# Kernel optimization log

Hardware: AMD Instinct MI355X
Metric: run time of the kernel (lower is better)

## Reference

```python
import jax, jax.numpy as jnp
import numpy as np

N, E, B = 10000, 160000, 64
ND, ED, H, L, C = 128, 64, 256, 4, 10
LN_EPS = 1e-5


def _layernorm(x, g, b):
    mu = jnp.mean(x, axis=-1, keepdims=True)
    var = jnp.mean(jnp.square(x - mu), axis=-1, keepdims=True)
    return (x - mu) * jax.lax.rsqrt(var + LN_EPS) * g + b


def setup_inputs() -> dict:
    key = jax.random.key(0)
    ks = jax.random.split(key, 24)

    def w(k, shape, fan_in):
        return jax.random.normal(k, shape, jnp.float32) * (1.0 / np.sqrt(fan_in))

    node_features = jax.random.normal(ks[0], (N, ND), jnp.float32)
    edge_index = jax.random.randint(ks[1], (2, E), 0, N, jnp.int64)
    edge_features = jax.random.normal(ks[2], (E, ED), jnp.float32)
    # deterministic sorted batch assignment (no empty graphs)
    batch = (jnp.arange(N, dtype=jnp.int64) * B) // N

    inp = dict(
        node_features=node_features,
        edge_index=edge_index,
        edge_features=edge_features,
        batch=batch,
        node_W=w(ks[3], (ND, H), ND), node_b=jnp.zeros((H,), jnp.float32),
        edge_W=w(ks[4], (ED, H), ED), edge_b=jnp.zeros((H,), jnp.float32),
        msg_W1=w(ks[5], (L, 3 * H, H), 3 * H), msg_b1=jnp.zeros((L, H), jnp.float32),
        msg_W2=w(ks[6], (L, H, H), H), msg_b2=jnp.zeros((L, H), jnp.float32),
        upd_W1=w(ks[7], (L, 2 * H, H), 2 * H), upd_b1=jnp.zeros((L, H), jnp.float32),
        upd_W2=w(ks[8], (L, H, H), H), upd_b2=jnp.zeros((L, H), jnp.float32),
        ln_g=jnp.ones((L, H), jnp.float32), ln_b=jnp.zeros((L, H), jnp.float32),
        ro_W1=w(ks[9], (H, H), H), ro_b1=jnp.zeros((H,), jnp.float32),
        ro_W2=w(ks[10], (H, C), H), ro_b2=jnp.zeros((C,), jnp.float32),
    )
    return inp


def _forward(node_features, edge_features, node_W, node_b, edge_W, edge_b,
             msg_W1, msg_b1, msg_W2, msg_b2, upd_W1, upd_b1, upd_W2, upd_b2,
             ln_g, ln_b, ro_W1, ro_b1, ro_W2, ro_b2, edge_index, batch):
    src, dst = edge_index[0], edge_index[1]
    x = node_features @ node_W + node_b            # [N, H]
    edge_attr = edge_features @ edge_W + edge_b    # [E, H]
    for l in range(L):
        # batched gather-MLP over all edges (vectorized version of the per-edge loop)
        m_in = jnp.concatenate([x[src], x[dst], edge_attr], axis=-1)  # [E, 3H]
        msg = jax.nn.relu(m_in @ msg_W1[l] + msg_b1[l]) @ msg_W2[l] + msg_b2[l]
        agg = jnp.zeros_like(x).at[dst].add(msg)    # scatter-add by destination
        u_in = jnp.concatenate([x, agg], axis=-1)   # [N, 2H]
        upd = jax.nn.relu(u_in @ upd_W1[l] + upd_b1[l]) @ upd_W2[l] + upd_b2[l]
        x = _layernorm(x + upd, ln_g[l], ln_b[l])
    # global mean pool per graph
    sums = jax.ops.segment_sum(x, batch, num_segments=B)
    cnts = jax.ops.segment_sum(jnp.ones((x.shape[0], 1), x.dtype), batch, num_segments=B)
    pooled = sums / cnts                            # [B, H]
    return jax.nn.relu(pooled @ ro_W1 + ro_b1) @ ro_W2 + ro_b2  # [B, C]


def reference(node_features, edge_index, edge_features, batch,
              node_W, node_b, edge_W, edge_b,
              msg_W1, msg_b1, msg_W2, msg_b2,
              upd_W1, upd_b1, upd_W2, upd_b2,
              ln_g, ln_b, ro_W1, ro_b1, ro_W2, ro_b2):
    return _forward(node_features, edge_features, node_W, node_b, edge_W, edge_b,
                    msg_W1, msg_b1, msg_W2, msg_b2, upd_W1, upd_b1, upd_W2, upd_b2,
                    ln_g, ln_b, ro_W1, ro_b1, ro_W2, ro_b2, edge_index, batch)
```

## Files before the change

kernel.cpp:

```cpp
#include <hip/hip_runtime.h>
#include <cstdint>
#include <cstddef>


typedef unsigned short u16;
typedef __attribute__((ext_vector_type(4))) float f32x4;
typedef __attribute__((ext_vector_type(8))) short bf16x8;
typedef __attribute__((ext_vector_type(4))) short s16x4;

constexpr int kN  = 10000;
constexpr int kE  = 160000;
constexpr int kB  = 64;
constexpr int kH  = 256;
constexpr int kL  = 4;
constexpr int kC  = 10;
constexpr float kEps = 1e-5f;

struct __align__(16) F4 { float v[4]; };
__device__ __forceinline__ F4 ldF4(const float* p) { return *reinterpret_cast<const F4*>(p); }

__device__ __forceinline__ u16 f2bf(float f) {
    unsigned u = __builtin_bit_cast(unsigned, f);
    return (u16)((u + 0x7fffu + ((u >> 16) & 1u)) >> 16);
}
__device__ __forceinline__ float bf2f(u16 h) {
    return __builtin_bit_cast(float, (unsigned)h << 16);
}

typedef __attribute__((address_space(1))) void GV;
typedef __attribute__((address_space(3))) void LV;
__device__ __forceinline__ void gl_lds16(const void* g, void* l) {
    __builtin_amdgcn_global_load_lds((GV*)g, (LV*)l, 16, 0, 0);
}
__device__ __forceinline__ void dma_w16k(const u16* __restrict__ Wc, char* lds, int tid) {
    const int w = tid >> 6, lane = tid & 63;
    char* lb = lds + w * 4096;
    const char* gb = (const char*)Wc + w * 4096 + lane * 16;
    #pragma unroll
    for (int i = 0; i < 4; ++i) gl_lds16(gb + i * 1024, lb + i * 1024);
}

__global__ void k_detect_i64(const unsigned* __restrict__ w, int* __restrict__ flag) {
    if (threadIdx.x == 0 && blockIdx.x == 0) {
        int is64 = 1;
        for (int i = 0; i < 64; ++i)
            if (w[2*i + 1] != 0u) { is64 = 0; break; }
        *flag = is64;
    }
}
__global__ void k_cvt_idx(const unsigned* __restrict__ w, const int* __restrict__ flag,
                          int* __restrict__ out, int n) {
    int i = blockIdx.x * 256 + threadIdx.x;
    if (i < n) out[i] = (*flag) ? (int)w[2*i] : (int)w[i];
}

__global__ __launch_bounds__(256) void k_hist(const int* __restrict__ dst,
                                              int* __restrict__ cnt) {
    int e = blockIdx.x * 256 + threadIdx.x;
    if (e < kE) atomicAdd(&cnt[dst[e]], 1);
}
__global__ __launch_bounds__(256) void k_scan(const int* __restrict__ cnt,
                                              int* __restrict__ cur) {
    __shared__ int part[256];
    const int t = threadIdx.x;
    const int per = (kN + 255) / 256;
    int s = 0;
    for (int i = 0; i < per; ++i) {
        int idx = t * per + i;
        if (idx < kN) s += cnt[idx];
    }
    int own = s;
    part[t] = s; __syncthreads();
    for (int off = 1; off < 256; off <<= 1) {
        int v = (t >= off) ? part[t - off] : 0;
        __syncthreads();
        part[t] += v;
        __syncthreads();
    }
    int run = part[t] - own;
    for (int i = 0; i < per; ++i) {
        int idx = t * per + i;
        if (idx < kN) { cur[idx] = run; run += cnt[idx]; }
    }
}
__global__ __launch_bounds__(256) void k_scatter(
    const int* __restrict__ src, const int* __restrict__ dst,
    int* __restrict__ cur, int* __restrict__ perm,
    int* __restrict__ ssorted, int* __restrict__ dsorted) {
    int e = blockIdx.x * 256 + threadIdx.x;
    if (e < kE) {
        int d = dst[e];
        int p = atomicAdd(&cur[d], 1);
        perm[p] = e;
        ssorted[p] = src[e];
        dsorted[p] = d;
    }
}

__global__ __launch_bounds__(256) void k_prep_w(
    const float* __restrict__ mW1, const float* __restrict__ mW2,
    const float* __restrict__ uW1, const float* __restrict__ uW2,
    u16* __restrict__ tm1, u16* __restrict__ tm2,
    u16* __restrict__ tu1, u16* __restrict__ tu2)
{
    int idx = blockIdx.x * 256 + threadIdx.x;
    const int S1 = kL * 768 * 256;
    const int S2 = S1 + kL * 256 * 256;
    const int S3 = S2 + kL * 512 * 256;
    const int S4 = S3 + kL * 256 * 256;
    const float* src; u16* dst; int K, r;
    if (idx < S1)      { src = mW1; dst = tm1; K = 768; r = idx; }
    else if (idx < S2) { src = mW2; dst = tm2; K = 256; r = idx - S1; }
    else if (idx < S3) { src = uW1; dst = tu1; K = 512; r = idx - S2; }
    else if (idx < S4) { src = uW2; dst = tu2; K = 256; r = idx - S3; }
    else return;
    int per = K * 256;
    int layer = r / per, rr = r - layer * per;
    int k = rr >> 8, n = rr & 255;
    int kc = k >> 5, kg = (k >> 3) & 3, e = k & 7;
    dst[(size_t)layer * per + (size_t)kc * 8192 + n * 32 + ((kg ^ ((n >> 1) & 3)) << 3) + e]
        = f2bf(src[(size_t)layer * per + rr]);
}

__global__ __launch_bounds__(256) void k_prep_m(
    const float* __restrict__ eW, const float* __restrict__ eb,
    const float* __restrict__ mW1, const float* __restrict__ mb1,
    u16* __restrict__ tmc, float* __restrict__ b1p)
{
    __shared__ float sWe[16 * 256];
    const int l = blockIdx.x, rq = blockIdx.y, t = threadIdx.x;
    const int r0 = rq * 16;
    #pragma unroll
    for (int i = 0; i < 16; ++i) sWe[i * 256 + t] = eW[(size_t)(r0 + i) * 256 + t];
    __syncthreads();
    const float* W1c = mW1 + (size_t)l * 768 * 256 + (size_t)512 * 256;
    float m[16];
    #pragma unroll
    for (int r = 0; r < 16; ++r) m[r] = 0.f;
    float bp = (rq == 0) ? mb1[l * 256 + t] : 0.f;
    for (int j = 0; j < 256; ++j) {
        float wv = W1c[(size_t)j * 256 + t];
        if (rq == 0) bp = fmaf(eb[j], wv, bp);
        #pragma unroll
        for (int r = 0; r < 16; ++r) m[r] = fmaf(sWe[r * 256 + j], wv, m[r]);
    }
    if (rq == 0) b1p[l * 256 + t] = bp;
    #pragma unroll
    for (int r = 0; r < 16; ++r) {
        int k = r0 + r;
        int kc = k >> 5, kg = (k >> 3) & 3, e = k & 7;
        tmc[(size_t)l * 16384 + (size_t)kc * 8192 + t * 32
            + ((kg ^ ((t >> 1) & 3)) << 3) + e] = f2bf(m[r]);
    }
}

__global__ __launch_bounds__(256) void k_encode_nodes(
    const float* __restrict__ nf, const float* __restrict__ W,
    const float* __restrict__ b, float* __restrict__ x, u16* __restrict__ x_bf)
{
    __shared__ float s_nf[4 * 128];
    const int n0 = blockIdx.x * 4;
    const int tid = threadIdx.x;
    reinterpret_cast<float2*>(s_nf)[tid] =
        reinterpret_cast<const float2*>(nf + (size_t)n0 * 128)[tid];
    __syncthreads();
    float acc[4] = {0.f, 0.f, 0.f, 0.f};
    for (int k = 0; k < 128; ++k) {
        float w = W[k * kH + tid];
        #pragma unroll
        for (int r = 0; r < 4; ++r) acc[r] = fmaf(s_nf[r * 128 + k], w, acc[r]);
    }
    float bias = b[tid];
    #pragma unroll
    for (int r = 0; r < 4; ++r) {
        float o = acc[r] + bias;
        x[(size_t)(n0 + r) * kH + tid] = o;
        x_bf[(size_t)(n0 + r) * kH + tid] = f2bf(o);
    }
}

__device__ __forceinline__ bf16x8 rdfrag(const char* lds, int n, int kg) {
    return *reinterpret_cast<const bf16x8*>(lds + n * 64 + ((kg ^ ((n >> 1) & 3)) << 4));
}
__device__ __forceinline__ bf16x8 rdH(const char* H, int row, int kbyte) {
    return *reinterpret_cast<const bf16x8*>(H + row * 512 + (kbyte ^ ((row & 7) << 4)));
}

__global__ __launch_bounds__(256, 3) void k_node_pre(
    const u16* __restrict__ x_bf, const u16* __restrict__ Wt1,
    u16* __restrict__ y_a, u16* __restrict__ y_b)
{
    __shared__ char sWt[16384];
    __shared__ char sA[4096];
    const int tid = threadIdx.x;
    const int n0 = blockIdx.x * 64;
    const int half = blockIdx.y;
    const u16* Wt = Wt1 + (size_t)half * 8 * 8192;
    u16* y = half ? y_b : y_a;
    const int w = tid >> 6, lane = tid & 63;
    const int lr = lane & 15, lg = lane >> 4;
    const int srow = tid >> 2, skg = tid & 3;
    const int kg_src = skg ^ ((srow >> 1) & 3);
    int gnode = n0 + srow; if (gnode >= kN) gnode = kN - 1;

    f32x4 acc[4][4];
    #pragma unroll
    for (int i = 0; i < 4; ++i)
        #pragma unroll
        for (int j = 0; j < 4; ++j) acc[i][j] = (f32x4){0.f, 0.f, 0.f, 0.f};

    for (int kc = 0; kc < 8; ++kc) {
        __syncthreads();
        dma_w16k(Wt + (size_t)kc * 8192, sWt, tid);
        gl_lds16(x_bf + (size_t)gnode * kH + kc * 32 + kg_src * 8, sA + w * 1024);
        __syncthreads();
        bf16x8 af[4], bfm[4];
        #pragma unroll
        for (int i = 0; i < 4; ++i) af[i] = rdfrag(sWt, w * 64 + i * 16 + lr, lg);
        #pragma unroll
        for (int j = 0; j < 4; ++j) bfm[j] = rdfrag(sA, j * 16 + lr, lg);
        #pragma unroll
        for (int i = 0; i < 4; ++i)
            #pragma unroll
            for (int j = 0; j < 4; ++j)
                acc[i][j] = __builtin_amdgcn_mfma_f32_16x16x32_bf16(af[i], bfm[j], acc[i][j], 0, 0, 0);
    }
    #pragma unroll
    for (int i = 0; i < 4; ++i) {
        const int hc0 = w * 64 + i * 16 + lg * 4;
        #pragma unroll
        for (int j = 0; j < 4; ++j) {
            const int node = n0 + j * 16 + lr;
            if (node < kN) {
                s16x4 o;
                #pragma unroll
                for (int q = 0; q < 4; ++q) o[q] = (short)f2bf(acc[i][j][q]);
                *reinterpret_cast<s16x4*>(y + (size_t)node * kH + hc0) = o;
            }
        }
    }
}

__global__ __launch_bounds__(256, 3) void k_msg(
    const float* __restrict__ ef,
    const int* __restrict__ ssorted, const int* __restrict__ dsorted,
    const int* __restrict__ perm,
    const u16* __restrict__ y_a, const u16* __restrict__ y_b,
    const u16* __restrict__ Wtm, const float* __restrict__ b1p,
    const u16* __restrict__ Wt2, const float* __restrict__ b2,
    float* __restrict__ agg)
{
    __shared__ char sWt[16384];
    __shared__ char sA[4096];
    __shared__ char sH[32768];
    __shared__ int sDst[64];

    const int tid = threadIdx.x;
    const int nwg = gridDim.x;
    const int q8 = nwg >> 3, r8 = nwg & 7;
    const int xcd = blockIdx.x & 7, sub = blockIdx.x >> 3;
    const int bid = (xcd < r8 ? xcd * (q8 + 1) : r8 * (q8 + 1) + (xcd - r8) * q8) + sub;
    const int e0 = bid * 64;

    const int w = tid >> 6, lane = tid & 63;
    const int lr = lane & 15, lg = lane >> 4;
    const int srow = tid >> 2, skg = tid & 3;

    const int my_src  = ssorted[e0 + srow];
    const int my_dst  = dsorted[e0 + srow];
    const int my_perm = perm[e0 + srow];
    if (tid < 64) sDst[tid] = dsorted[e0 + tid];

    #pragma unroll
    for (int m = 0; m < 8; ++m) {
        int col0 = skg * 8 + m * 32;
        bf16x8 va = *reinterpret_cast<const bf16x8*>(y_a + (size_t)my_src * kH + col0);
        bf16x8 vb = *reinterpret_cast<const bf16x8*>(y_b + (size_t)my_dst * kH + col0);
        bf16x8 o;
        #pragma unroll
        for (int t = 0; t < 8; ++t)
            o[t] = (short)f2bf(bf2f((u16)va[t]) + bf2f((u16)vb[t]));
        int byte = srow * 512 + col0 * 2;
        *reinterpret_cast<bf16x8*>(sH + (byte ^ ((srow & 7) << 4))) = o;
    }

    f32x4 acc[4][4];
    #pragma unroll
    for (int i = 0; i < 4; ++i)
        #pragma unroll
        for (int j = 0; j < 4; ++j) acc[i][j] = (f32x4){0.f, 0.f, 0.f, 0.f};

    for (int kc = 0; kc < 2; ++kc) {
        __syncthreads();
        dma_w16k(Wtm + (size_t)kc * 8192, sWt, tid);
        {
            const float* ap = ef + (size_t)my_perm * 64 + kc * 32 + skg * 8;
            F4 a0 = ldF4(ap), a1 = ldF4(ap + 4);
            int4 bv;
            bv.x = (int)f2bf(a0.v[0]) | ((int)f2bf(a0.v[1]) << 16);
            bv.y = (int)f2bf(a0.v[2]) | ((int)f2bf(a0.v[3]) << 16);
            bv.z = (int)f2bf(a1.v[0]) | ((int)f2bf(a1.v[1]) << 16);
            bv.w = (int)f2bf(a1.v[2]) | ((int)f2bf(a1.v[3]) << 16);
            *reinterpret_cast<int4*>(sA + srow * 64 + ((skg ^ ((srow >> 1) & 3)) << 4)) = bv;
        }
        __syncthreads();
        bf16x8 af[4], bfm[4];
        #pragma unroll
        for (int i = 0; i < 4; ++i) af[i] = rdfrag(sWt, w * 64 + i * 16 + lr, lg);
        #pragma unroll
        for (int j = 0; j < 4; ++j) bfm[j] = rdfrag(sA, j * 16 + lr, lg);
        #pragma unroll
        for (int i = 0; i < 4; ++i)
            #pragma unroll
            for (int j = 0; j < 4; ++j)
                acc[i][j] = __builtin_amdgcn_mfma_f32_16x16x32_bf16(af[i], bfm[j], acc[i][j], 0, 0, 0);
    }

    #pragma unroll
    for (int i = 0; i < 4; ++i) {
        const int hc0 = w * 64 + i * 16 + lg * 4;
        const F4 bb = ldF4(b1p + hc0);
        #pragma unroll
        for (int j = 0; j < 4; ++j) {
            const int edge = j * 16 + lr;
            int addr = (edge * 512 + hc0 * 2) ^ ((edge & 7) << 4);
            s16x4 ys = *reinterpret_cast<const s16x4*>(sH + addr);
            s16x4 o;
            #pragma unroll
            for (int q = 0; q < 4; ++q) {
                float h = acc[i][j][q] + bb.v[q] + bf2f((u16)ys[q]);
                h = h > 0.f ? h : 0.f;
                o[q] = (short)f2bf(h);
            }
            *reinterpret_cast<s16x4*>(sH + addr) = o;
            acc[i][j] = (f32x4){0.f, 0.f, 0.f, 0.f};
        }
    }

    for (int kc = 0; kc < 8; ++kc) {
        __syncthreads();
        dma_w16k(Wt2 + (size_t)kc * 8192, sWt, tid);
        __syncthreads();
        bf16x8 af2[4], bf2[4];
        #pragma unroll
        for (int i = 0; i < 4; ++i) af2[i] = rdH(sH, i * 16 + lr, kc * 64 + lg * 16);
        #pragma unroll
        for (int j = 0; j < 4; ++j) bf2[j] = rdfrag(sWt, w * 64 + j * 16 + lr, lg);
        #pragma unroll
        for (int i = 0; i < 4; ++i)
            #pragma unroll
            for (int j = 0; j < 4; ++j)
                acc[i][j] = __builtin_amdgcn_mfma_f32_16x16x32_bf16(af2[i], bf2[j], acc[i][j], 0, 0, 0);
    }

    __syncthreads();
    #pragma unroll
    for (int j = 0; j < 4; ++j) {
        const int oc = w * 64 + j * 16 + lr;
        const float b2v = b2[oc];
        #pragma unroll
        for (int i = 0; i < 4; ++i)
            #pragma unroll
            for (int q = 0; q < 4; ++q) {
                int edge = i * 16 + lg * 4 + q;
                int byte = edge * 512 + oc * 2;
                *reinterpret_cast<u16*>(sH + (byte ^ ((edge & 7) << 4)))
                    = f2bf(acc[i][j][q] + b2v);
            }
    }
    __syncthreads();

    {
        const int col = tid;
        float run = 0.f;
        int prev = sDst[0];
        #pragma unroll 1
        for (int eb = 0; eb < 8; ++eb) {
            float vv[8]; int dd[8];
            #pragma unroll
            for (int t = 0; t < 8; ++t) {
                int e = eb * 8 + t;
                int byte = e * 512 + col * 2;
                vv[t] = bf2f(*reinterpret_cast<const u16*>(sH + (byte ^ ((e & 7) << 4))));
                dd[t] = sDst[e];
            }
            #pragma unroll
            for (int t = 0; t < 8; ++t) {
                if (dd[t] != prev) {
                    unsafeAtomicAdd(agg + (size_t)prev * kH + col, run);
                    run = 0.f; prev = dd[t];
                }
                run += vv[t];
            }
        }
        unsafeAtomicAdd(agg + (size_t)prev * kH + col, run);
    }
}

__global__ __launch_bounds__(256, 2) void k_upd(
    float* __restrict__ x, u16* __restrict__ x_bf,
    float* __restrict__ agg,
    const u16* __restrict__ Wt1, const float* __restrict__ b1,
    const u16* __restrict__ Wt2, const float* __restrict__ b2,
    const float* __restrict__ lng, const float* __restrict__ lnb)
{
    __shared__ char sWt[2][16384];
    __shared__ char sA[2][4096];
    __shared__ char sH[32768];

    const int tid = threadIdx.x;
    const int n0 = blockIdx.x * 64;
    const int w = tid >> 6, lane = tid & 63;
    const int lr = lane & 15, lg = lane >> 4;
    const int srow = tid >> 2, skg = tid & 3;
    const int kg_src = skg ^ ((srow >> 1) & 3);
    int gnode = n0 + srow; if (gnode >= kN) gnode = kN - 1;

    dma_w16k(Wt1, sWt[0], tid);
    gl_lds16(x_bf + (size_t)gnode * kH + kg_src * 8, sA[0] + w * 1024);

    f32x4 acc[4][4];
    #pragma unroll
    for (int i = 0; i < 4; ++i)
        #pragma unroll
        for (int j = 0; j < 4; ++j) acc[i][j] = (f32x4){0.f, 0.f, 0.f, 0.f};
    __syncthreads();

    for (int kc = 0; kc < 16; ++kc) {
        const int cur = kc & 1, nxt = cur ^ 1;
        bool do_agg = false; F4 a0, a1;
        if (kc < 15) {
            dma_w16k(Wt1 + (size_t)(kc + 1) * 8192, sWt[nxt], tid);
            if (kc + 1 < 8) {
                gl_lds16(x_bf + (size_t)gnode * kH + (kc + 1) * 32 + kg_src * 8,
                         sA[nxt] + w * 1024);
            } else {
                const float* ap = agg + (size_t)gnode * kH + (kc + 1 - 8) * 32 + skg * 8;
                a0 = ldF4(ap); a1 = ldF4(ap + 4); do_agg = true;
            }
        } else {
            dma_w16k(Wt2, sWt[nxt], tid);
        }
        bf16x8 af[4], bfm[4];
        #pragma unroll
        for (int i = 0; i < 4; ++i) af[i] = rdfrag(sWt[cur], w * 64 + i * 16 + lr, lg);
        #pragma unroll
        for (int j = 0; j < 4; ++j) bfm[j] = rdfrag(sA[cur], j * 16 + lr, lg);
        #pragma unroll
        for (int i = 0; i < 4; ++i)
            #pragma unroll
            for (int j = 0; j < 4; ++j)
                acc[i][j] = __builtin_amdgcn_mfma_f32_16x16x32_bf16(af[i], bfm[j], acc[i][j], 0, 0, 0);
        if (do_agg) {
            int4 bv;
            bv.x = (int)f2bf(a0.v[0]) | ((int)f2bf(a0.v[1]) << 16);
            bv.y = (int)f2bf(a0.v[2]) | ((int)f2bf(a0.v[3]) << 16);
            bv.z = (int)f2bf(a1.v[0]) | ((int)f2bf(a1.v[1]) << 16);
            bv.w = (int)f2bf(a1.v[2]) | ((int)f2bf(a1.v[3]) << 16);
            *reinterpret_cast<int4*>(sA[nxt] + srow * 64 + ((skg ^ ((srow >> 1) & 3)) << 4)) = bv;
        }
        __syncthreads();
    }

    #pragma unroll
    for (int i = 0; i < 4; ++i) {
        const int hc0 = w * 64 + i * 16 + lg * 4;
        const F4 bb = ldF4(b1 + hc0);
        #pragma unroll
        for (int j = 0; j < 4; ++j) {
            const int row = j * 16 + lr;
            s16x4 o;
            #pragma unroll
            for (int q = 0; q < 4; ++q) {
                float h = acc[i][j][q] + bb.v[q];
                h = h > 0.f ? h : 0.f;
                o[q] = (short)f2bf(h);
            }
            int byte = row * 512 + hc0 * 2;
            *reinterpret_cast<s16x4*>(sH + (byte ^ ((row & 7) << 4))) = o;
            acc[i][j] = (f32x4){0.f, 0.f, 0.f, 0.f};
        }
    }
    __syncthreads();

    {
        float4 z = make_float4(0.f, 0.f, 0.f, 0.f);
        float4* bp = reinterpret_cast<float4*>(agg + (size_t)n0 * kH);
        #pragma unroll
        for (int i = 0; i < 16; ++i) {
            int idx = i * 256 + tid;
            int row = idx >> 6;
            if (n0 + row < kN) bp[idx] = z;
        }
    }

    for (int kc = 0; kc < 8; ++kc) {
        const int cur = kc & 1, nxt = cur ^ 1;
        if (kc < 7) dma_w16k(Wt2 + (size_t)(kc + 1) * 8192, sWt[nxt], tid);
        bf16x8 af2[4], bf2[4];
        #pragma unroll
        for (int i = 0; i < 4; ++i) af2[i] = rdH(sH, i * 16 + lr, kc * 64 + lg * 16);
        #pragma unroll
        for (int j = 0; j < 4; ++j) bf2[j] = rdfrag(sWt[cur], w * 64 + j * 16 + lr, lg);
        #pragma unroll
        for (int i = 0; i < 4; ++i)
            #pragma unroll
            for (int j = 0; j < 4; ++j)
                acc[i][j] = __builtin_amdgcn_mfma_f32_16x16x32_bf16(af2[i], bf2[j], acc[i][j], 0, 0, 0);
        __syncthreads();
    }

    float b2v[4], gv[4], bvn[4];
    #pragma unroll
    for (int j = 0; j < 4; ++j) {
        int oc = w * 64 + j * 16 + lr;
        b2v[j] = b2[oc]; gv[j] = lng[oc]; bvn[j] = lnb[oc];
    }
    #pragma unroll
    for (int i = 0; i < 4; ++i)
        #pragma unroll
        for (int j = 0; j < 4; ++j) {
            int oc = w * 64 + j * 16 + lr;
            #pragma unroll
            for (int q = 0; q < 4; ++q) {
                int node = n0 + i * 16 + lg * 4 + q;
                int ncl = node < kN ? node : kN - 1;
                acc[i][j][q] += b2v[j] + x[(size_t)ncl * kH + oc];
            }
        }

    float (*red)[64][2] = reinterpret_cast<float(*)[64][2]>(sA[0]);
    float2* mstd = reinterpret_cast<float2*>(sA[0] + 2048);
    __syncthreads();
    #pragma unroll
    for (int i = 0; i < 4; ++i)
        #pragma unroll
        for (int q = 0; q < 4; ++q) {
            float s = acc[i][0][q] + acc[i][1][q] + acc[i][2][q] + acc[i][3][q];
            float ss = acc[i][0][q] * acc[i][0][q] + acc[i][1][q] * acc[i][1][q]
                     + acc[i][2][q] * acc[i][2][q] + acc[i][3][q] * acc[i][3][q];
            #pragma unroll
            for (int m = 1; m < 16; m <<= 1) { s += __shfl_xor(s, m); ss += __shfl_xor(ss, m); }
            if (lr == 0) { red[w][i * 16 + lg * 4 + q][0] = s; red[w][i * 16 + lg * 4 + q][1] = ss; }
        }
    __syncthreads();
    if (tid < 64) {
        float s = red[0][tid][0] + red[1][tid][0] + red[2][tid][0] + red[3][tid][0];
        float ss = red[0][tid][1] + red[1][tid][1] + red[2][tid][1] + red[3][tid][1];
        float mean = s * (1.f / 256.f);
        float var = ss * (1.f / 256.f) - mean * mean;
        mstd[tid] = make_float2(mean, rsqrtf(var + kEps));
    }
    __syncthreads();
    #pragma unroll
    for (int i = 0; i < 4; ++i)
        #pragma unroll
        for (int j = 0; j < 4; ++j) {
            int oc = w * 64 + j * 16 + lr;
            #pragma unroll
            for (int q = 0; q < 4; ++q) {
                int nn = i * 16 + lg * 4 + q;
                int node = n0 + nn;
                if (node < kN) {
                    float2 ms = mstd[nn];
                    float o = (acc[i][j][q] - ms.x) * ms.y * gv[j] + bvn[j];
                    x[(size_t)node * kH + oc] = o;
                    x_bf[(size_t)node * kH + oc] = f2bf(o);
                }
            }
        }
}

__device__ __forceinline__ int lower_bound_i(const int* a, int n, int v) {
    int lo = 0, hi = n;
    while (lo < hi) { int m = (lo + hi) >> 1; if (a[m] < v) lo = m + 1; else hi = m; }
    return lo;
}

__global__ __launch_bounds__(256) void k_pool_ro(
    const float* __restrict__ x, const int* __restrict__ batch,
    const float* __restrict__ W1, const float* __restrict__ b1,
    const float* __restrict__ W2, const float* __restrict__ b2,
    float* __restrict__ out)
{
    __shared__ float ph[kH];
    __shared__ float h1[kH];
    const int b = blockIdx.x, t = threadIdx.x;
    const int s = lower_bound_i(batch, kN, b);
    const int e = lower_bound_i(batch, kN, b + 1);
    float acc = 0.f;
    for (int i = s; i < e; ++i) acc += x[(size_t)i * kH + t];
    ph[t] = acc / (float)(e - s);
    __syncthreads();
    float a = b1[t];
    for (int k = 0; k < kH; ++k) a = fmaf(ph[k], W1[k * kH + t], a);
    h1[t] = a > 0.f ? a : 0.f;
    __syncthreads();
    if (t < kC) {
        float o = b2[t];
        for (int k = 0; k < kH; ++k) o = fmaf(h1[k], W2[k * kC + t], o);
        out[b * kC + t] = o;
    }
}

extern "C" void kernel_launch(void* const* d_in, const int* in_sizes, int n_in,
                              void* d_out, int out_size, void* d_ws, size_t ws_size,
                              hipStream_t stream)
{
    const float* nf     = (const float*)d_in[0];
    const void*  ei_raw = d_in[1];
    const float* ef     = (const float*)d_in[2];
    const void*  ba_raw = d_in[3];
    const float* node_W = (const float*)d_in[4];
    const float* node_b = (const float*)d_in[5];
    const float* edge_W = (const float*)d_in[6];
    const float* edge_b = (const float*)d_in[7];
    const float* msg_W1 = (const float*)d_in[8];
    const float* msg_b1 = (const float*)d_in[9];
    const float* msg_W2 = (const float*)d_in[10];
    const float* msg_b2 = (const float*)d_in[11];
    const float* upd_W1 = (const float*)d_in[12];
    const float* upd_b1 = (const float*)d_in[13];
    const float* upd_W2 = (const float*)d_in[14];
    const float* upd_b2 = (const float*)d_in[15];
    const float* ln_g   = (const float*)d_in[16];
    const float* ln_b   = (const float*)d_in[17];
    const float* ro_W1  = (const float*)d_in[18];
    const float* ro_b1  = (const float*)d_in[19];
    const float* ro_W2  = (const float*)d_in[20];
    const float* ro_b2  = (const float*)d_in[21];

    char* p = (char*)d_ws;
    auto alloc = [&](size_t bytes) { char* r = p; p += (bytes + 255) & ~(size_t)255; return r; };
    float* x    = (float*)alloc((size_t)kN * kH * 4);
    float* agg  = (float*)alloc((size_t)kN * kH * 4);
    u16* x_bf   = (u16*)alloc((size_t)kN * kH * 2);
    u16* y_a    = (u16*)alloc((size_t)kN * kH * 2);
    u16* y_b    = (u16*)alloc((size_t)kN * kH * 2);
    u16* tm1 = (u16*)alloc((size_t)kL * 768 * 256 * 2);
    u16* tm2 = (u16*)alloc((size_t)kL * 256 * 256 * 2);
    u16* tu1 = (u16*)alloc((size_t)kL * 512 * 256 * 2);
    u16* tu2 = (u16*)alloc((size_t)kL * 256 * 256 * 2);
    u16* tmc = (u16*)alloc((size_t)kL * 64 * 256 * 2);
    float* b1p = (float*)alloc((size_t)kL * 256 * 4);
    int* ei32 = (int*)alloc((size_t)2 * kE * 4);
    int* ba32 = (int*)alloc((size_t)kN * 4);
    int* cnt  = (int*)alloc((size_t)kN * 4);
    int* cur  = (int*)alloc((size_t)kN * 4);
    int* perm = (int*)alloc((size_t)kE * 4);
    int* ssorted = (int*)alloc((size_t)kE * 4);
    int* dsorted = (int*)alloc((size_t)kE * 4);
    int* flag = (int*)alloc(4);

    k_detect_i64<<<1, 64, 0, stream>>>((const unsigned*)ei_raw, flag);
    k_cvt_idx<<<(2 * kE + 255) / 256, 256, 0, stream>>>((const unsigned*)ei_raw, flag, ei32, 2 * kE);
    k_cvt_idx<<<(kN + 255) / 256, 256, 0, stream>>>((const unsigned*)ba_raw, flag, ba32, kN);
    const int* src = ei32;
    const int* dst = ei32 + kE;

    hipMemsetAsync(cnt, 0, (size_t)kN * 4, stream);
    k_hist<<<(kE + 255) / 256, 256, 0, stream>>>(dst, cnt);
    k_scan<<<1, 256, 0, stream>>>(cnt, cur);
    k_scatter<<<(kE + 255) / 256, 256, 0, stream>>>(src, dst, cur, perm, ssorted, dsorted);

    const int prep_elems = kL * (768 + 256 + 512 + 256) * 256;
    k_prep_w<<<(prep_elems + 255) / 256, 256, 0, stream>>>(
        msg_W1, msg_W2, upd_W1, upd_W2, tm1, tm2, tu1, tu2);
    k_prep_m<<<dim3(kL, 4), 256, 0, stream>>>(edge_W, edge_b, msg_W1, msg_b1, tmc, b1p);

    k_encode_nodes<<<kN / 4, 256, 0, stream>>>(nf, node_W, node_b, x, x_bf);

    hipMemsetAsync(agg, 0, (size_t)kN * kH * sizeof(float), stream);
    for (int l = 0; l < kL; ++l) {
        k_node_pre<<<dim3((kN + 63) / 64, 2), 256, 0, stream>>>(
            x_bf, tm1 + (size_t)l * 768 * 256, y_a, y_b);
        k_msg<<<kE / 64, 256, 0, stream>>>(ef, ssorted, dsorted, perm, y_a, y_b,
            tmc + (size_t)l * 64 * 256, b1p + l * 256,
            tm2 + (size_t)l * 256 * 256, msg_b2 + l * kH, agg);
        k_upd<<<(kN + 63) / 64, 256, 0, stream>>>(x, x_bf, agg,
            tu1 + (size_t)l * 512 * 256, upd_b1 + l * kH,
            tu2 + (size_t)l * 256 * 256, upd_b2 + l * kH,
            ln_g + l * kH, ln_b + l * kH);
    }

    k_pool_ro<<<kB, 256, 0, stream>>>(x, ba32, ro_W1, ro_b1, ro_W2, ro_b2, (float*)d_out);
}
```

Measured before the change: 608.7 us.

## Fuse next-layer node projection into update kernel and pre-permute edge features

The per-layer k_node_pre launch is folded into k_upd: after the layernorm it keeps the new bf16 node rows in LDS and computes y_a/y_b for the next layer, double-buffering weights. Edge features are permuted and converted to swizzled bf16 once in a new prep kernel, so k_msg loads them with a direct global-to-LDS DMA. k_msg now gathers y_a/y_b straight into registers in the epilogue rather than staging them through LDS. Packed v_cvt_pk_bf16_f32 conversions replace the manual rounding. The cost is longer, more register-hungry k_upd blocks, a small extra numeric difference from hardware bf16 rounding, and a one-time permute pass.

```diff
diff --git a/kernel.cpp b/kernel.cpp
--- a/kernel.cpp
+++ b/kernel.cpp
@@ -25,6 +25,11 @@
 }
 __device__ __forceinline__ float bf2f(u16 h) {
     return __builtin_bit_cast(float, (unsigned)h << 16);
+}
+__device__ __forceinline__ unsigned cvtpk(float lo, float hi) {
+    unsigned r;
+    asm("v_cvt_pk_bf16_f32 %0, %1, %2" : "=v"(r) : "v"(lo), "v"(hi));
+    return r;
 }
 
 typedef __attribute__((address_space(1))) void GV;
@@ -122,6 +127,20 @@
         = f2bf(src[(size_t)layer * per + rr]);
 }
 
+__global__ __launch_bounds__(256) void k_prep_ef(
+    const float* __restrict__ ef, const int* __restrict__ perm,
+    u16* __restrict__ efs)
+{
+    int idx = blockIdx.x * 256 + threadIdx.x;
+    if (idx >= kE * 64) return;
+    int p = idx >> 6, k = idx & 63;
+    float v = ef[(size_t)perm[p] * 64 + k];
+    int row = p & 63, blk = p >> 6;
+    int kc = k >> 5, kg = (k >> 3) & 3, e = k & 7;
+    efs[(size_t)blk * 4096 + kc * 2048 + row * 32
+        + ((kg ^ ((row >> 1) & 3)) << 3) + e] = f2bf(v);
+}
+
 __global__ __launch_bounds__(256) void k_prep_m(
     const float* __restrict__ eW, const float* __restrict__ eb,
     const float* __restrict__ mW1, const float* __restrict__ mb1,
@@ -232,19 +251,18 @@
         for (int j = 0; j < 4; ++j) {
             const int node = n0 + j * 16 + lr;
             if (node < kN) {
-                s16x4 o;
-                #pragma unroll
-                for (int q = 0; q < 4; ++q) o[q] = (short)f2bf(acc[i][j][q]);
-                *reinterpret_cast<s16x4*>(y + (size_t)node * kH + hc0) = o;
+                uint2 o;
+                o.x = cvtpk(acc[i][j][0], acc[i][j][1]);
+                o.y = cvtpk(acc[i][j][2], acc[i][j][3]);
+                *reinterpret_cast<uint2*>(y + (size_t)node * kH + hc0) = o;
             }
         }
     }
 }
 
 __global__ __launch_bounds__(256, 3) void k_msg(
-    const float* __restrict__ ef,
+    const u16* __restrict__ efs,
     const int* __restrict__ ssorted, const int* __restrict__ dsorted,
-    const int* __restrict__ perm,
     const u16* __restrict__ y_a, const u16* __restrict__ y_b,
     const u16* __restrict__ Wtm, const float* __restrict__ b1p,
     const u16* __restrict__ Wt2, const float* __restrict__ b2,
@@ -264,24 +282,13 @@
 
     const int w = tid >> 6, lane = tid & 63;
     const int lr = lane & 15, lg = lane >> 4;
-    const int srow = tid >> 2, skg = tid & 3;
-
-    const int my_src  = ssorted[e0 + srow];
-    const int my_dst  = dsorted[e0 + srow];
-    const int my_perm = perm[e0 + srow];
+
     if (tid < 64) sDst[tid] = dsorted[e0 + tid];
-
-    #pragma unroll
-    for (int m = 0; m < 8; ++m) {
-        int col0 = skg * 8 + m * 32;
-        bf16x8 va = *reinterpret_cast<const bf16x8*>(y_a + (size_t)my_src * kH + col0);
-        bf16x8 vb = *reinterpret_cast<const bf16x8*>(y_b + (size_t)my_dst * kH + col0);
-        bf16x8 o;
-        #pragma unroll
-        for (int t = 0; t < 8; ++t)
-            o[t] = (short)f2bf(bf2f((u16)va[t]) + bf2f((u16)vb[t]));
-        int byte = srow * 512 + col0 * 2;
-        *reinterpret_cast<bf16x8*>(sH + (byte ^ ((srow & 7) << 4))) = o;
+    int esrc[4], edst[4];
+    #pragma unroll
+    for (int j = 0; j < 4; ++j) {
+        esrc[j] = ssorted[e0 + j * 16 + lr];
+        edst[j] = dsorted[e0 + j * 16 + lr];
     }
 
     f32x4 acc[4][4];
@@ -293,16 +300,8 @@
     for (int kc = 0; kc < 2; ++kc) {
         __syncthreads();
         dma_w16k(Wtm + (size_t)kc * 8192, sWt, tid);
-        {
-            const float* ap = ef + (size_t)my_perm * 64 + kc * 32 + skg * 8;
-            F4 a0 = ldF4(ap), a1 = ldF4(ap + 4);
-            int4 bv;
-            bv.x = (int)f2bf(a0.v[0]) | ((int)f2bf(a0.v[1]) << 16);
-            bv.y = (int)f2bf(a0.v[2]) | ((int)f2bf(a0.v[3]) << 16);
-            bv.z = (int)f2bf(a1.v[0]) | ((int)f2bf(a1.v[1]) << 16);
-            bv.w = (int)f2bf(a1.v[2]) | ((int)f2bf(a1.v[3]) << 16);
-            *reinterpret_cast<int4*>(sA + srow * 64 + ((skg ^ ((srow >> 1) & 3)) << 4)) = bv;
-        }
+        gl_lds16((const char*)efs + (size_t)bid * 8192 + kc * 4096 + w * 1024 + lane * 16,
+                 sA + w * 1024);
         __syncthreads();
         bf16x8 af[4], bfm[4];
         #pragma unroll
@@ -317,25 +316,36 @@
     }
 
     #pragma unroll
-    for (int i = 0; i < 4; ++i) {
-        const int hc0 = w * 64 + i * 16 + lg * 4;
-        const F4 bb = ldF4(b1p + hc0);
-        #pragma unroll
-        for (int j = 0; j < 4; ++j) {
-            const int edge = j * 16 + lr;
-            int addr = (edge * 512 + hc0 * 2) ^ ((edge & 7) << 4);
-            s16x4 ys = *reinterpret_cast<const s16x4*>(sH + addr);
-            s16x4 o;
-            #pragma unroll
-            for (int q = 0; q < 4; ++q) {
-                float h = acc[i][j][q] + bb.v[q] + bf2f((u16)ys[q]);
-                h = h > 0.f ? h : 0.f;
-                o[q] = (short)f2bf(h);
-            }
-            *reinterpret_cast<s16x4*>(sH + addr) = o;
+    for (int j = 0; j < 4; ++j) {
+        const int edge = j * 16 + lr;
+        const u16* pa = y_a + (size_t)esrc[j] * kH;
+        const u16* pb = y_b + (size_t)edst[j] * kH;
+        uint2 ya[4], yb[4];
+        #pragma unroll
+        for (int i = 0; i < 4; ++i) {
+            const int hc0 = w * 64 + i * 16 + lg * 4;
+            ya[i] = *reinterpret_cast<const uint2*>(pa + hc0);
+            yb[i] = *reinterpret_cast<const uint2*>(pb + hc0);
+        }
+        #pragma unroll
+        for (int i = 0; i < 4; ++i) {
+            const int hc0 = w * 64 + i * 16 + lg * 4;
+            const F4 bb = ldF4(b1p + hc0);
+            float s0 = __builtin_bit_cast(float, ya[i].x << 16) + __builtin_bit_cast(float, yb[i].x << 16);
+            float s1 = __builtin_bit_cast(float, ya[i].x & 0xffff0000u) + __builtin_bit_cast(float, yb[i].x & 0xffff0000u);
+            float s2 = __builtin_bit_cast(float, ya[i].y << 16) + __builtin_bit_cast(float, yb[i].y << 16);
+            float s3 = __builtin_bit_cast(float, ya[i].y & 0xffff0000u) + __builtin_bit_cast(float, yb[i].y & 0xffff0000u);
+            float h0 = acc[i][j][0] + bb.v[0] + s0; h0 = h0 > 0.f ? h0 : 0.f;
+            float h1 = acc[i][j][1] + bb.v[1] + s1; h1 = h1 > 0.f ? h1 : 0.f;
+            float h2 = acc[i][j][2] + bb.v[2] + s2; h2 = h2 > 0.f ? h2 : 0.f;
+            float h3 = acc[i][j][3] + bb.v[3] + s3; h3 = h3 > 0.f ? h3 : 0.f;
+            uint2 o; o.x = cvtpk(h0, h1); o.y = cvtpk(h2, h3);
+            int byte = edge * 512 + hc0 * 2;
+            *reinterpret_cast<uint2*>(sH + (byte ^ ((edge & 7) << 4))) = o;
             acc[i][j] = (f32x4){0.f, 0.f, 0.f, 0.f};
         }
     }
+    __syncthreads();
 
     for (int kc = 0; kc < 8; ++kc) {
         __syncthreads();
@@ -359,14 +369,15 @@
         const int oc = w * 64 + j * 16 + lr;
         const float b2v = b2[oc];
         #pragma unroll
-        for (int i = 0; i < 4; ++i)
-            #pragma unroll
-            for (int q = 0; q < 4; ++q) {
-                int edge = i * 16 + lg * 4 + q;
-                int byte = edge * 512 + oc * 2;
-                *reinterpret_cast<u16*>(sH + (byte ^ ((edge & 7) << 4)))
-                    = f2bf(acc[i][j][q] + b2v);
-            }
+        for (int i = 0; i < 4; ++i) {
+            unsigned p01 = cvtpk(acc[i][j][0] + b2v, acc[i][j][1] + b2v);
+            unsigned p23 = cvtpk(acc[i][j][2] + b2v, acc[i][j][3] + b2v);
+            int eb0 = i * 16 + lg * 4;
+            *reinterpret_cast<u16*>(sH + (((eb0 + 0) * 512 + oc * 2) ^ (((eb0 + 0) & 7) << 4))) = (u16)p01;
+            *reinterpret_cast<u16*>(sH + (((eb0 + 1) * 512 + oc * 2) ^ (((eb0 + 1) & 7) << 4))) = (u16)(p01 >> 16);
+            *reinterpret_cast<u16*>(sH + (((eb0 + 2) * 512 + oc * 2) ^ (((eb0 + 2) & 7) << 4))) = (u16)p23;
+            *reinterpret_cast<u16*>(sH + (((eb0 + 3) * 512 + oc * 2) ^ (((eb0 + 3) & 7) << 4))) = (u16)(p23 >> 16);
+        }
     }
     __syncthreads();
 
@@ -402,7 +413,9 @@
     float* __restrict__ agg,
     const u16* __restrict__ Wt1, const float* __restrict__ b1,
     const u16* __restrict__ Wt2, const float* __restrict__ b2,
-    const float* __restrict__ lng, const float* __restrict__ lnb)
+    const float* __restrict__ lng, const float* __restrict__ lnb,
+    const u16* __restrict__ Wt1n, int do_y,
+    u16* __restrict__ y_a, u16* __restrict__ y_b)
 {
     __shared__ char sWt[2][16384];
     __shared__ char sA[2][4096];
@@ -453,10 +466,10 @@
                 acc[i][j] = __builtin_amdgcn_mfma_f32_16x16x32_bf16(af[i], bfm[j], acc[i][j], 0, 0, 0);
         if (do_agg) {
             int4 bv;
-            bv.x = (int)f2bf(a0.v[0]) | ((int)f2bf(a0.v[1]) << 16);
-            bv.y = (int)f2bf(a0.v[2]) | ((int)f2bf(a0.v[3]) << 16);
-            bv.z = (int)f2bf(a1.v[0]) | ((int)f2bf(a1.v[1]) << 16);
-            bv.w = (int)f2bf(a1.v[2]) | ((int)f2bf(a1.v[3]) << 16);
+            bv.x = (int)cvtpk(a0.v[0], a0.v[1]);
+            bv.y = (int)cvtpk(a0.v[2], a0.v[3]);
+            bv.z = (int)cvtpk(a1.v[0], a1.v[1]);
+            bv.w = (int)cvtpk(a1.v[2], a1.v[3]);
             *reinterpret_cast<int4*>(sA[nxt] + srow * 64 + ((skg ^ ((srow >> 1) & 3)) << 4)) = bv;
         }
         __syncthreads();
@@ -469,15 +482,13 @@
         #pragma unroll
         for (int j = 0; j < 4; ++j) {
             const int row = j * 16 + lr;
-            s16x4 o;
-            #pragma unroll
-            for (int q = 0; q < 4; ++q) {
-                float h = acc[i][j][q] + bb.v[q];
-                h = h > 0.f ? h : 0.f;
-                o[q] = (short)f2bf(h);
-            }
+            float h0 = acc[i][j][0] + bb.v[0]; h0 = h0 > 0.f ? h0 : 0.f;
+            float h1 = acc[i][j][1] + bb.v[1]; h1 = h1 > 0.f ? h1 : 0.f;
+            float h2 = acc[i][j][2] + bb.v[2]; h2 = h2 > 0.f ? h2 : 0.f;
+            float h3 = acc[i][j][3] + bb.v[3]; h3 = h3 > 0.f ? h3 : 0.f;
+            uint2 o; o.x = cvtpk(h0, h1); o.y = cvtpk(h2, h3);
             int byte = row * 512 + hc0 * 2;
-            *reinterpret_cast<s16x4*>(sH + (byte ^ ((row & 7) << 4))) = o;
+            *reinterpret_cast<uint2*>(sH + (byte ^ ((row & 7) << 4))) = o;
             acc[i][j] = (f32x4){0.f, 0.f, 0.f, 0.f};
         }
     }
@@ -564,11 +575,59 @@
                 if (node < kN) {
                     float2 ms = mstd[nn];
                     float o = (acc[i][j][q] - ms.x) * ms.y * gv[j] + bvn[j];
+                    u16 ob = f2bf(o);
                     x[(size_t)node * kH + oc] = o;
-                    x_bf[(size_t)node * kH + oc] = f2bf(o);
+                    x_bf[(size_t)node * kH + oc] = ob;
+                    if (do_y) {
+                        int byte = nn * 512 + oc * 2;
+                        *reinterpret_cast<u16*>(sH + (byte ^ ((nn & 7) << 4))) = ob;
+                    }
                 }
             }
         }
+
+    if (do_y) {
+        __syncthreads();
+        dma_w16k(Wt1n, sWt[0], tid);
+        #pragma unroll
+        for (int i = 0; i < 4; ++i)
+            #pragma unroll
+            for (int j = 0; j < 4; ++j) acc[i][j] = (f32x4){0.f, 0.f, 0.f, 0.f};
+        __syncthreads();
+        for (int c = 0; c < 16; ++c) {
+            const int cur = c & 1;
+            if (c < 15) dma_w16k(Wt1n + (size_t)(c + 1) * 8192, sWt[cur ^ 1], tid);
+            bf16x8 af[4], bfm[4];
+            #pragma unroll
+            for (int i = 0; i < 4; ++i) af[i] = rdfrag(sWt[cur], w * 64 + i * 16 + lr, lg);
+            #pragma unroll
+            for (int j = 0; j < 4; ++j) bfm[j] = rdH(sH, j * 16 + lr, (c & 7) * 64 + lg * 16);
+            #pragma unroll
+            for (int i = 0; i < 4; ++i)
+                #pragma unroll
+                for (int j = 0; j < 4; ++j)
+                    acc[i][j] = __builtin_amdgcn_mfma_f32_16x16x32_bf16(af[i], bfm[j], acc[i][j], 0, 0, 0);
+            if (c == 7 || c == 15) {
+                u16* y = (c == 7) ? y_a : y_b;
+                #pragma unroll
+                for (int i = 0; i < 4; ++i) {
+                    const int hc0 = w * 64 + i * 16 + lg * 4;
+                    #pragma unroll
+                    for (int j = 0; j < 4; ++j) {
+                        const int node = n0 + j * 16 + lr;
+                        if (node < kN) {
+                            uint2 o;
+                            o.x = cvtpk(acc[i][j][0], acc[i][j][1]);
+                            o.y = cvtpk(acc[i][j][2], acc[i][j][3]);
+                            *reinterpret_cast<uint2*>(y + (size_t)node * kH + hc0) = o;
+                        }
+                        acc[i][j] = (f32x4){0.f, 0.f, 0.f, 0.f};
+                    }
+                }
+            }
+            __syncthreads();
+        }
+    }
 }
 
 __device__ __forceinline__ int lower_bound_i(const int* a, int n, int v) {
@@ -637,6 +696,7 @@
     u16* x_bf   = (u16*)alloc((size_t)kN * kH * 2);
     u16* y_a    = (u16*)alloc((size_t)kN * kH * 2);
     u16* y_b    = (u16*)alloc((size_t)kN * kH * 2);
+    u16* efs    = (u16*)alloc((size_t)kE * 64 * 2);
     u16* tm1 = (u16*)alloc((size_t)kL * 768 * 256 * 2);
     u16* tm2 = (u16*)alloc((size_t)kL * 256 * 256 * 2);
     u16* tu1 = (u16*)alloc((size_t)kL * 512 * 256 * 2);
@@ -667,20 +727,23 @@
     k_prep_w<<<(prep_elems + 255) / 256, 256, 0, stream>>>(
         msg_W1, msg_W2, upd_W1, upd_W2, tm1, tm2, tu1, tu2);
     k_prep_m<<<dim3(kL, 4), 256, 0, stream>>>(edge_W, edge_b, msg_W1, msg_b1, tmc, b1p);
+    k_prep_ef<<<(kE * 64 + 255) / 256, 256, 0, stream>>>(ef, perm, efs);
 
     k_encode_nodes<<<kN / 4, 256, 0, stream>>>(nf, node_W, node_b, x, x_bf);
 
     hipMemsetAsync(agg, 0, (size_t)kN * kH * sizeof(float), stream);
+    k_node_pre<<<dim3((kN + 63) / 64, 2), 256, 0, stream>>>(x_bf, tm1, y_a, y_b);
+
     for (int l = 0; l < kL; ++l) {
-        k_node_pre<<<dim3((kN + 63) / 64, 2), 256, 0, stream>>>(
-            x_bf, tm1 + (size_t)l * 768 * 256, y_a, y_b);
-        k_msg<<<kE / 64, 256, 0, stream>>>(ef, ssorted, dsorted, perm, y_a, y_b,
+        k_msg<<<kE / 64, 256, 0, stream>>>(efs, ssorted, dsorted, y_a, y_b,
             tmc + (size_t)l * 64 * 256, b1p + l * 256,
             tm2 + (size_t)l * 256 * 256, msg_b2 + l * kH, agg);
+        const int do_y = (l < kL - 1) ? 1 : 0;
         k_upd<<<(kN + 63) / 64, 256, 0, stream>>>(x, x_bf, agg,
             tu1 + (size_t)l * 512 * 256, upd_b1 + l * kH,
             tu2 + (size_t)l * 256 * 256, upd_b2 + l * kH,
-            ln_g + l * kH, ln_b + l * kH);
+            ln_g + l * kH, ln_b + l * kH,
+            tm1 + (size_t)(l + 1 < kL ? l + 1 : 0) * 768 * 256, do_y, y_a, y_b);
     }
 
     k_pool_ro<<<kB, 256, 0, stream>>>(x, ba32, ro_W1, ro_b1, ro_W2, ro_b2, (float*)d_out);
```

New measurement: 658.6 us. 8.2% more time.
